# Kernel tuning notes

Hardware: AMD Instinct MI355X
Metric: run time of the kernel (lower is better)

## Reference

```python
import jax, jax.numpy as jnp
import numpy as np

THETA = 10000.0


def _rope_tables(T, head_dim, dtype):
    # w = 1/theta^(arange(1, d+1, 2)[:d//2] / d); positions start at 1 (matches source)
    exps = jnp.arange(1, head_dim + 1, 2, dtype=jnp.float32)[: head_dim // 2] / head_dim
    w = 1.0 / (THETA ** exps)
    t = jnp.arange(1, T + 1, dtype=jnp.float32)
    angles = t[:, None] * w[None, :]  # [T, d/2]
    return jnp.sin(angles).astype(dtype), jnp.cos(angles).astype(dtype)


def _rotate(x, sin, cos):
    # x: [..., T, d], sin/cos: [T, d/2]; rotate interleaved len-2 subvectors
    x1 = x[..., ::2]
    x2 = x[..., 1::2]
    x1p = x1 * cos - x2 * sin
    x2p = x1 * sin + x2 * cos
    return jnp.stack((x1p, x2p), axis=-1).reshape(x.shape)


def setup_inputs() -> dict:
    key = jax.random.key(0)
    B, Tq, Tkv, C = 4, 2048, 2048, 1024
    k1, k2, k3, k4, k5 = jax.random.split(key, 5)
    s = 1.0 / np.sqrt(C)
    return {
        "x_q": jax.random.normal(k1, (B, Tq, C), dtype=jnp.float32),
        "x_kv": jax.random.normal(k2, (B, Tkv, C), dtype=jnp.float32),
        "q_tok_mask": jnp.ones((B, Tq), dtype=bool),
        "kv_tok_mask": jnp.ones((B, Tkv), dtype=bool),
        "W_q": jax.random.normal(k3, (C, C), dtype=jnp.float32) * s,
        "W_kv": jax.random.normal(k4, (C, 2 * C), dtype=jnp.float32) * s,
        "W_c": jax.random.normal(k5, (C, C), dtype=jnp.float32) * s,
    }


def reference(x_q, x_kv, q_tok_mask, kv_tok_mask, W_q, W_kv, W_c):
    B, Tq, C = x_q.shape
    Tkv = x_kv.shape[1]
    H = 16
    D = C // H  # head_dim = 64

    q = (x_q @ W_q).reshape(B, Tq, H, D).transpose(0, 2, 1, 3)      # [B,H,Tq,D]
    kv = x_kv @ W_kv                                                  # [B,Tkv,2C]
    k, v = kv[..., :C], kv[..., C:]
    k = k.reshape(B, Tkv, H, D).transpose(0, 2, 1, 3)                 # [B,H,Tkv,D]
    v = v.reshape(B, Tkv, H, D).transpose(0, 2, 1, 3)

    sin_q, cos_q = _rope_tables(Tq, D, x_q.dtype)
    sin_k, cos_k = _rope_tables(Tkv, D, x_q.dtype)
    q = _rotate(q, sin_q, cos_q)
    k = _rotate(k, sin_k, cos_k)

    att = jnp.einsum("bhqd,bhkd->bhqk", q, k) / jnp.sqrt(jnp.asarray(D, x_q.dtype))
    mask = (q_tok_mask[:, :, None] & kv_tok_mask[:, None, :])[:, None, :, :]  # [B,1,Tq,Tkv]
    att = jnp.where(mask, att, jnp.asarray(-1e9, att.dtype))
    att = jax.nn.softmax(att, axis=-1)

    y = jnp.einsum("bhqk,bhkd->bhqd", att, v)                         # [B,H,Tq,D]
    y = y.transpose(0, 2, 1, 3).reshape(B, Tq, C)
    return y @ W_c
```

## Files before the change

kernel.cpp:

```cpp
#include <hip/hip_runtime.h>
#include <hip/hip_bf16.h>
#include <math.h>

typedef float f32x4 __attribute__((ext_vector_type(4)));
typedef short bf16x8 __attribute__((ext_vector_type(8)));

#define DEVINL __device__ __forceinline__

DEVINL unsigned short f2bf(float f) {
  unsigned int u = __float_as_uint(f);
  return (unsigned short)((u + 0x7FFFu + ((u >> 16) & 1u)) >> 16);
}
DEVINL float bf2f(unsigned short h) { return __uint_as_float(((unsigned int)h) << 16); }

DEVINL unsigned int pack_bf2(float f0, float f1) {
  unsigned int u0 = __float_as_uint(f0) + 0x8000u;
  unsigned int u1 = __float_as_uint(f1) + 0x8000u;
#if __has_builtin(__builtin_amdgcn_perm)
  return __builtin_amdgcn_perm(u1, u0, 0x07060302u);
#else
  return (u0 >> 16) | (u1 & 0xffff0000u);
#endif
}

DEVINL float fast_exp2(float x) {
#if __has_builtin(__builtin_amdgcn_exp2f)
  return __builtin_amdgcn_exp2f(x);
#else
  return exp2f(x);
#endif
}

DEVINL void glds16(const unsigned short* g, unsigned short* l) {
  __builtin_amdgcn_global_load_lds(
      (const __attribute__((address_space(1))) void*)g,
      (__attribute__((address_space(3))) void*)l, 16, 0, 0);
}

__global__ void cvt2(const float* __restrict__ a, const float* __restrict__ b,
                     unsigned short* __restrict__ da, unsigned short* __restrict__ db,
                     int n8half) {
  int halfgrid = gridDim.x >> 1;
  int hi = blockIdx.x >= halfgrid;
  const float* src = hi ? b : a;
  unsigned short* dst = hi ? db : da;
  int bx = blockIdx.x - (hi ? halfgrid : 0);
  int stride = halfgrid * blockDim.x;
  for (int i = bx * blockDim.x + threadIdx.x; i < n8half; i += stride) {
    float4 x = ((const float4*)src)[2*i];
    float4 y = ((const float4*)src)[2*i + 1];
    union { unsigned short us[8]; uint4 v; } u;
    u.us[0]=f2bf(x.x); u.us[1]=f2bf(x.y); u.us[2]=f2bf(x.z); u.us[3]=f2bf(x.w);
    u.us[4]=f2bf(y.x); u.us[5]=f2bf(y.y); u.us[6]=f2bf(y.z); u.us[7]=f2bf(y.w);
    ((uint4*)dst)[i] = u.v;
  }
}

__global__ void transpose3(const float* __restrict__ Wq, const float* __restrict__ Wkv,
                           const float* __restrict__ Wc,
                           unsigned short* __restrict__ dq, unsigned short* __restrict__ dkv,
                           unsigned short* __restrict__ dc) {
  __shared__ float tile[32][33];
  int bx = blockIdx.x;
  const float* src; unsigned short* dst; int N;
  if (bx < 32)      { src = Wq;  dst = dq;  N = 1024; }
  else if (bx < 96) { src = Wkv; dst = dkv; N = 2048; bx -= 32; }
  else              { src = Wc;  dst = dc;  N = 1024; bx -= 96; }
  const int K = 1024;
  int n0 = bx * 32, k0 = blockIdx.y * 32;
  int tx = threadIdx.x, ty = threadIdx.y;
  for (int i = 0; i < 4; ++i) {
    int k = ty + i * 8;
    tile[k][tx] = src[(long)(k0 + k) * N + n0 + tx];
  }
  __syncthreads();
  for (int i = 0; i < 4; ++i) {
    int n = ty + i * 8;
    dst[(long)(n0 + n) * K + k0 + tx] = f2bf(tile[tx][n]);
  }
}

struct GemmCtx {
  int lane, lo16, quad, wm, wn;
  int r0, soff, ldsoff, fc;
};
DEVINL void gemm_core(const unsigned short* __restrict__ A, const unsigned short* __restrict__ Bt,
                      int m0, int n0, int K,
                      unsigned short* As, unsigned short* Bs,
                      const GemmCtx& c, f32x4 acc[4][4]) {
  int aoff[4], boff[4];
  for (int mt = 0; mt < 4; ++mt) aoff[mt] = (c.wm * 64 + mt * 16 + c.lo16) * 32 + c.fc;
  for (int nt = 0; nt < 4; ++nt) boff[nt] = (c.wn * 64 + nt * 16 + c.lo16) * 32 + c.fc;
  for (int k0 = 0; k0 < K; k0 += 32) {
    glds16(A  + (long)(m0 + c.r0)      * K + k0 + c.soff, As + c.ldsoff);
    glds16(A  + (long)(m0 + 64 + c.r0) * K + k0 + c.soff, As + 2048 + c.ldsoff);
    glds16(Bt + (long)(n0 + c.r0)      * K + k0 + c.soff, Bs + c.ldsoff);
    glds16(Bt + (long)(n0 + 64 + c.r0) * K + k0 + c.soff, Bs + 2048 + c.ldsoff);
    __syncthreads();
    bf16x8 af[4], bfv[4];
    for (int mt = 0; mt < 4; ++mt) af[mt]  = *(const bf16x8*)(As + aoff[mt]);
    for (int nt = 0; nt < 4; ++nt) bfv[nt] = *(const bf16x8*)(Bs + boff[nt]);
    for (int mt = 0; mt < 4; ++mt)
      for (int nt = 0; nt < 4; ++nt)
        acc[mt][nt] = __builtin_amdgcn_mfma_f32_16x16x32_bf16(af[mt], bfv[nt], acc[mt][nt], 0, 0, 0);
    __syncthreads();
  }
}
DEVINL GemmCtx make_ctx(int tid) {
  GemmCtx c;
  int wave = tid >> 6; c.lane = tid & 63;
  c.lo16 = c.lane & 15; c.quad = c.lane >> 4;
  c.wm = wave >> 1; c.wn = wave & 1;
  c.r0 = wave * 16 + (c.lane >> 2);
  c.soff = ((c.lane & 3) ^ ((c.lane >> 3) & 3)) * 8;
  c.ldsoff = wave * 512 + c.lane * 8;
  c.fc = (c.quad ^ ((c.lo16 >> 1) & 3)) * 8;
  return c;
}

__global__ __launch_bounds__(256) void gemm_qkv(
    const unsigned short* __restrict__ xq, const unsigned short* __restrict__ xkv,
    const unsigned short* __restrict__ wq, const unsigned short* __restrict__ wkv,
    unsigned short* __restrict__ qout, unsigned short* __restrict__ kout,
    unsigned short* __restrict__ vout, float qscale) {
  __shared__ unsigned short As[128 * 32];
  __shared__ unsigned short Bs[128 * 32];
  const bool isq = blockIdx.x < 8;
  const unsigned short* A  = isq ? xq : xkv;
  const unsigned short* Bt = isq ? wq : wkv;
  const int n0 = (isq ? blockIdx.x : (blockIdx.x - 8)) * 128;
  const int m0 = blockIdx.y * 128;
  GemmCtx c = make_ctx(threadIdx.x);
  f32x4 acc[4][4];
  f32x4 zero = {0.f, 0.f, 0.f, 0.f};
  for (int i = 0; i < 4; ++i) for (int j = 0; j < 4; ++j) acc[i][j] = zero;
  gemm_core(A, Bt, m0, n0, 1024, As, Bs, c, acc);

  const bool isv = (!isq) && (n0 >= 1024);
  const float LOG2_10000_64 = 0.20762050593046f;

  if (!isv) {
    unsigned short* out = isq ? qout : kout;
    const float scale = isq ? qscale : 1.0f;
    const float sgn = (c.lo16 & 1) ? 1.0f : -1.0f;
    for (int nt = 0; nt < 4; ++nt) {
      int gn = n0 + c.wn * 64 + nt * 16 + c.lo16;
      int d = gn & 63, h = gn >> 6;
      float w = fast_exp2(-(float)(2 * (d >> 1) + 1) * LOG2_10000_64);
      for (int mt = 0; mt < 4; ++mt) {
        int gmb = m0 + c.wm * 64 + mt * 16 + c.quad * 4;
        for (int r = 0; r < 4; ++r) {
          int gm = gmb + r;
          int b = gm >> 11, t = gm & 2047;
          float v = acc[mt][nt][r];
          float p = __shfl_xor(v, 1, 64);
          float sa, ca; __sincosf((float)(t + 1) * w, &sa, &ca);
          float res = fmaf(p, sgn * sa, v * ca) * scale;
          out[((long)((b * 16 + h) * 2048 + t)) * 64 + d] = f2bf(res);
        }
      }
    }
  } else {
    for (int mt = 0; mt < 4; ++mt) {
      int gmb = m0 + c.wm * 64 + mt * 16 + c.quad * 4;
      for (int nt = 0; nt < 4; ++nt) {
        int gn = n0 + c.wn * 64 + nt * 16 + c.lo16 - 1024;
        int h = gn >> 6, d = gn & 63;
        for (int r = 0; r < 4; ++r) {
          int gm = gmb + r;
          int b = gm >> 11, t = gm & 2047;
          int u = t & 31;
          int tp = (t & ~31) | (8 * ((u >> 2) & 3) + (u & 3) + 4 * (u >> 4));
          vout[((long)((b * 16 + h) * 64 + d)) * 2048 + tp] = f2bf(acc[mt][nt][r]);
        }
      }
    }
  }
}

__global__ __launch_bounds__(256) void gemm_out(
    const unsigned short* __restrict__ A, const unsigned short* __restrict__ Bt,
    float* __restrict__ out) {
  __shared__ unsigned short As[128 * 32];
  __shared__ unsigned short Bs[128 * 32];
  const int m0 = blockIdx.y * 128, n0 = blockIdx.x * 128;
  GemmCtx c = make_ctx(threadIdx.x);
  f32x4 acc[4][4];
  f32x4 zero = {0.f, 0.f, 0.f, 0.f};
  for (int i = 0; i < 4; ++i) for (int j = 0; j < 4; ++j) acc[i][j] = zero;
  gemm_core(A, Bt, m0, n0, 1024, As, Bs, c, acc);
  for (int mt = 0; mt < 4; ++mt) {
    int gmb = m0 + c.wm * 64 + mt * 16 + c.quad * 4;
    for (int nt = 0; nt < 4; ++nt) {
      int gn = n0 + c.wn * 64 + nt * 16 + c.lo16;
      for (int r = 0; r < 4; ++r)
        out[(long)(gmb + r) * 1024 + gn] = acc[mt][nt][r];
    }
  }
}

__global__ __launch_bounds__(128, 2) void flash_st(
    const unsigned short* __restrict__ Q, const unsigned short* __restrict__ Kr,
    const unsigned short* __restrict__ Vt, unsigned short* __restrict__ Y) {
  __shared__ unsigned short Ks[64 * 64];
  __shared__ unsigned short Vs[64 * 64];
  const int tid  = threadIdx.x;
  const int wave = tid >> 6, lane = tid & 63;
  const int lo16 = lane & 15, quad = lane >> 4;
  const int bh = blockIdx.x, b = bh >> 4, h = bh & 15;
  const int q0 = blockIdx.y * 128 + wave * 64;

  bf16x8 qf[4][2];
  for (int qt = 0; qt < 4; ++qt)
    for (int dk = 0; dk < 2; ++dk)
      qf[qt][dk] = *(const bf16x8*)(Q + ((long)bh * 2048 + q0 + qt * 16 + lo16) * 64 + dk * 32 + quad * 8);

  f32x4 zero = {0.f, 0.f, 0.f, 0.f};
  f32x4 o[4][4];
  f32x4 lacc[4];
  for (int dt = 0; dt < 4; ++dt) for (int qt = 0; qt < 4; ++qt) o[dt][qt] = zero;
  for (int qt = 0; qt < 4; ++qt) lacc[qt] = zero;

  const int sr = lane >> 3;
  const int gc = ((lane & 7) ^ sr) * 8;

  for (int kb = 0; kb < 2048; kb += 64) {
    for (int p = 0; p < 4; ++p) {
      int g = p * 2 + wave;
      int r = g * 8 + sr;
      glds16(Kr + ((long)bh * 2048 + kb + r) * 64 + gc, Ks + g * 512 + lane * 8);
      glds16(Vt + ((long)bh * 64 + r) * 2048 + kb + gc, Vs + g * 512 + lane * 8);
    }
    __syncthreads();

    for (int ks = 0; ks < 2; ++ks) {
      unsigned int p2[2][4][2];
      for (int ktl = 0; ktl < 2; ++ktl) {
        const int krow = (ks * 2 + ktl) * 16 + lo16;
        const int x7 = krow & 7;
        bf16x8 ka0 = *(const bf16x8*)(Ks + krow * 64 + ((quad ^ x7) * 8));
        bf16x8 ka1 = *(const bf16x8*)(Ks + krow * 64 + (((4 + quad) ^ x7) * 8));
        for (int qt = 0; qt < 4; ++qt) {
          f32x4 s = zero;
          s = __builtin_amdgcn_mfma_f32_16x16x32_bf16(ka0, qf[qt][0], s, 0, 0, 0);
          s = __builtin_amdgcn_mfma_f32_16x16x32_bf16(ka1, qf[qt][1], s, 0, 0, 0);
          f32x4 e;
          e[0] = fast_exp2(s[0]); e[1] = fast_exp2(s[1]);
          e[2] = fast_exp2(s[2]); e[3] = fast_exp2(s[3]);
          lacc[qt] += e;
          p2[ktl][qt][0] = pack_bf2(e[0], e[1]);
          p2[ktl][qt][1] = pack_bf2(e[2], e[3]);
        }
      }
      for (int dt = 0; dt < 4; ++dt) {
        const int vrow = dt * 16 + lo16;
        bf16x8 va = *(const bf16x8*)(Vs + vrow * 64 + (((ks * 4 + quad) ^ (vrow & 7)) * 8));
        for (int qt = 0; qt < 4; ++qt) {
          union { unsigned int u[4]; bf16x8 v; } pb;
          pb.u[0] = p2[0][qt][0]; pb.u[1] = p2[0][qt][1];
          pb.u[2] = p2[1][qt][0]; pb.u[3] = p2[1][qt][1];
          o[dt][qt] = __builtin_amdgcn_mfma_f32_16x16x32_bf16(va, pb.v, o[dt][qt], 0, 0, 0);
        }
      }
    }
    __syncthreads();
  }

  float rl[4];
  for (int qt = 0; qt < 4; ++qt) {
    float l = (lacc[qt][0] + lacc[qt][1]) + (lacc[qt][2] + lacc[qt][3]);
    l += __shfl_xor(l, 16, 64);
    l += __shfl_xor(l, 32, 64);
    rl[qt] = 1.0f / l;
  }

  for (int dt = 0; dt < 4; ++dt)
    for (int qt = 0; qt < 4; ++qt) {
      float v0 = o[dt][qt][0] * rl[qt], v1 = o[dt][qt][1] * rl[qt];
      float v2 = o[dt][qt][2] * rl[qt], v3 = o[dt][qt][3] * rl[qt];
      uint2 pk; pk.x = pack_bf2(v0, v1); pk.y = pack_bf2(v2, v3);
      long row = (long)b * 2048 + q0 + qt * 16 + lo16;
      int col = h * 64 + dt * 16 + quad * 4;
      *(uint2*)(Y + row * 1024 + col) = pk;
    }
}

extern "C" void kernel_launch(void* const* d_in, const int* in_sizes, int n_in,
                              void* d_out, int out_size, void* d_ws, size_t ws_size,
                              hipStream_t stream) {
  const float* x_q  = (const float*)d_in[0];
  const float* x_kv = (const float*)d_in[1];
  const float* W_q  = (const float*)d_in[4];
  const float* W_kv = (const float*)d_in[5];
  const float* W_c  = (const float*)d_in[6];

  char* ws = (char*)d_ws;
  const size_t MB = 1u << 20;
  unsigned short* xq_bf  = (unsigned short*)(ws + 0);
  unsigned short* xkv_bf = (unsigned short*)(ws + 16 * MB);
  unsigned short* wq_t   = (unsigned short*)(ws + 32 * MB);
  unsigned short* wkv_t  = (unsigned short*)(ws + 34 * MB);
  unsigned short* wc_t   = (unsigned short*)(ws + 38 * MB);
  unsigned short* q_r    = (unsigned short*)(ws + 40 * MB);
  unsigned short* k_r    = (unsigned short*)(ws + 56 * MB);
  unsigned short* v_t    = (unsigned short*)(ws + 72 * MB);
  unsigned short* y      = xq_bf;

  const float QSCALE = 0.125f * 1.44269504088896f;

  dim3 tb(32, 8);
  cvt2<<<2048, 256, 0, stream>>>(x_q, x_kv, xq_bf, xkv_bf, 1048576);
  transpose3<<<dim3(128, 32), tb, 0, stream>>>(W_q, W_kv, W_c, wq_t, wkv_t, wc_t);
  gemm_qkv<<<dim3(24, 64), 256, 0, stream>>>(xq_bf, xkv_bf, wq_t, wkv_t, q_r, k_r, v_t, QSCALE);
  flash_st<<<dim3(64, 16), 128, 0, stream>>>(q_r, k_r, v_t, y);
  gemm_out<<<dim3(8, 64), 256, 0, stream>>>(y, wc_t, (float*)d_out);
}
```

Baseline: 314.8 us.

## Double-buffer K/V tiles in flash attention with async prefetch and MFMA priority

Splits the K and V shared-memory tiles into two buffers and issues the loads for the next key block before computing the current one. Explicit vmcnt waits and raw barriers replace __syncthreads so global-to-LDS traffic can overlap the MFMA and exp work. It also raises wave priority around MFMA groups. The cost is twice the LDS, which may limit occupancy, and the hand-written vmcnt(8) must match the number of outstanding loads per stage.

```diff
diff --git a/kernel.cpp b/kernel.cpp
--- a/kernel.cpp
+++ b/kernel.cpp
@@ -202,8 +202,8 @@
 __global__ __launch_bounds__(128, 2) void flash_st(
     const unsigned short* __restrict__ Q, const unsigned short* __restrict__ Kr,
     const unsigned short* __restrict__ Vt, unsigned short* __restrict__ Y) {
-  __shared__ unsigned short Ks[64 * 64];
-  __shared__ unsigned short Vs[64 * 64];
+  __shared__ unsigned short Ks[2][64 * 64];
+  __shared__ unsigned short Vs[2][64 * 64];
   const int tid  = threadIdx.x;
   const int wave = tid >> 6, lane = tid & 63;
   const int lo16 = lane & 15, quad = lane >> 4;
@@ -223,27 +223,45 @@
 
   const int sr = lane >> 3;
   const int gc = ((lane & 7) ^ sr) * 8;
+  const unsigned short* Kg = Kr + (long)bh * 2048 * 64;
+  const unsigned short* Vg = Vt + (long)bh * 64 * 2048;
+
+#define STAGE_KV(KB, BI) do {                                            \
+    for (int p = 0; p < 4; ++p) {                                        \
+      int g = p * 2 + wave;                                              \
+      int r = g * 8 + sr;                                                \
+      glds16(Kg + (long)((KB) + r) * 64 + gc, &Ks[BI][g * 512 + lane * 8]); \
+      glds16(Vg + (long)r * 2048 + (KB) + gc, &Vs[BI][g * 512 + lane * 8]); \
+    } } while (0)
+
+  STAGE_KV(0, 0);
+  int buf = 0;
 
   for (int kb = 0; kb < 2048; kb += 64) {
-    for (int p = 0; p < 4; ++p) {
-      int g = p * 2 + wave;
-      int r = g * 8 + sr;
-      glds16(Kr + ((long)bh * 2048 + kb + r) * 64 + gc, Ks + g * 512 + lane * 8);
-      glds16(Vt + ((long)bh * 64 + r) * 2048 + kb + gc, Vs + g * 512 + lane * 8);
-    }
-    __syncthreads();
+    if (kb + 64 < 2048) {
+      STAGE_KV(kb + 64, buf ^ 1);
+      asm volatile("s_waitcnt vmcnt(8)" ::: "memory");
+    } else {
+      asm volatile("s_waitcnt vmcnt(0)" ::: "memory");
+    }
+    __builtin_amdgcn_s_barrier();
+    asm volatile("" ::: "memory");
+    const unsigned short* Kb = &Ks[buf][0];
+    const unsigned short* Vb = &Vs[buf][0];
 
     for (int ks = 0; ks < 2; ++ks) {
       unsigned int p2[2][4][2];
       for (int ktl = 0; ktl < 2; ++ktl) {
         const int krow = (ks * 2 + ktl) * 16 + lo16;
         const int x7 = krow & 7;
-        bf16x8 ka0 = *(const bf16x8*)(Ks + krow * 64 + ((quad ^ x7) * 8));
-        bf16x8 ka1 = *(const bf16x8*)(Ks + krow * 64 + (((4 + quad) ^ x7) * 8));
+        bf16x8 ka0 = *(const bf16x8*)(Kb + krow * 64 + ((quad ^ x7) * 8));
+        bf16x8 ka1 = *(const bf16x8*)(Kb + krow * 64 + (((4 + quad) ^ x7) * 8));
         for (int qt = 0; qt < 4; ++qt) {
           f32x4 s = zero;
+          __builtin_amdgcn_s_setprio(1);
           s = __builtin_amdgcn_mfma_f32_16x16x32_bf16(ka0, qf[qt][0], s, 0, 0, 0);
           s = __builtin_amdgcn_mfma_f32_16x16x32_bf16(ka1, qf[qt][1], s, 0, 0, 0);
+          __builtin_amdgcn_s_setprio(0);
           f32x4 e;
           e[0] = fast_exp2(s[0]); e[1] = fast_exp2(s[1]);
           e[2] = fast_exp2(s[2]); e[3] = fast_exp2(s[3]);
@@ -254,17 +272,22 @@
       }
       for (int dt = 0; dt < 4; ++dt) {
         const int vrow = dt * 16 + lo16;
-        bf16x8 va = *(const bf16x8*)(Vs + vrow * 64 + (((ks * 4 + quad) ^ (vrow & 7)) * 8));
+        bf16x8 va = *(const bf16x8*)(Vb + vrow * 64 + (((ks * 4 + quad) ^ (vrow & 7)) * 8));
+        __builtin_amdgcn_s_setprio(1);
         for (int qt = 0; qt < 4; ++qt) {
           union { unsigned int u[4]; bf16x8 v; } pb;
           pb.u[0] = p2[0][qt][0]; pb.u[1] = p2[0][qt][1];
           pb.u[2] = p2[1][qt][0]; pb.u[3] = p2[1][qt][1];
           o[dt][qt] = __builtin_amdgcn_mfma_f32_16x16x32_bf16(va, pb.v, o[dt][qt], 0, 0, 0);
         }
+        __builtin_amdgcn_s_setprio(0);
       }
     }
-    __syncthreads();
-  }
+    asm volatile("" ::: "memory");
+    __builtin_amdgcn_s_barrier();
+    buf ^= 1;
+  }
+#undef STAGE_KV
 
   float rl[4];
   for (int qt = 0; qt < 4; ++qt) {
```

Result: no change. 318.2 us (+1.1%).

## Load K/V fragments directly from global into registers, drop LDS staging

Applied to the files above, without the earlier changes.

The flash attention kernel no longer stages K and V tiles through shared memory with barriers. Each wave now loads its MFMA operand fragments straight from global memory into registers, relying on L2/L1 for reuse between the two waves. It also adds s_setprio around MFMA groups and removes the occupancy hint from launch_bounds. This removes LDS traffic and __syncthreads. The cost is duplicated global loads across waves, less coalesced access for the strided V reads, and higher register pressure.

```diff
diff --git a/kernel.cpp b/kernel.cpp
--- a/kernel.cpp
+++ b/kernel.cpp
@@ -199,17 +199,18 @@
   }
 }
 
-__global__ __launch_bounds__(128, 2) void flash_st(
+__global__ __launch_bounds__(128) void flash_st(
     const unsigned short* __restrict__ Q, const unsigned short* __restrict__ Kr,
     const unsigned short* __restrict__ Vt, unsigned short* __restrict__ Y) {
-  __shared__ unsigned short Ks[64 * 64];
-  __shared__ unsigned short Vs[64 * 64];
   const int tid  = threadIdx.x;
   const int wave = tid >> 6, lane = tid & 63;
   const int lo16 = lane & 15, quad = lane >> 4;
   const int bh = blockIdx.x, b = bh >> 4, h = bh & 15;
   const int q0 = blockIdx.y * 128 + wave * 64;
 
+  const unsigned short* Kg = Kr + (long)bh * 2048 * 64;
+  const unsigned short* Vg = Vt + (long)bh * 64 * 2048;
+
   bf16x8 qf[4][2];
   for (int qt = 0; qt < 4; ++qt)
     for (int dk = 0; dk < 2; ++dk)
@@ -221,29 +222,29 @@
   for (int dt = 0; dt < 4; ++dt) for (int qt = 0; qt < 4; ++qt) o[dt][qt] = zero;
   for (int qt = 0; qt < 4; ++qt) lacc[qt] = zero;
 
-  const int sr = lane >> 3;
-  const int gc = ((lane & 7) ^ sr) * 8;
+  const unsigned short* kp = Kg + (long)lo16 * 64 + quad * 8;
+  const unsigned short* vp = Vg + (long)lo16 * 2048 + quad * 8;
 
   for (int kb = 0; kb < 2048; kb += 64) {
-    for (int p = 0; p < 4; ++p) {
-      int g = p * 2 + wave;
-      int r = g * 8 + sr;
-      glds16(Kr + ((long)bh * 2048 + kb + r) * 64 + gc, Ks + g * 512 + lane * 8);
-      glds16(Vt + ((long)bh * 64 + r) * 2048 + kb + gc, Vs + g * 512 + lane * 8);
-    }
-    __syncthreads();
+    bf16x8 ka[4][2];
+    bf16x8 va[2][4];
+    for (int kt = 0; kt < 4; ++kt)
+      for (int hf = 0; hf < 2; ++hf)
+        ka[kt][hf] = *(const bf16x8*)(kp + (long)(kb + kt * 16) * 64 + hf * 32);
+    for (int ks = 0; ks < 2; ++ks)
+      for (int dt = 0; dt < 4; ++dt)
+        va[ks][dt] = *(const bf16x8*)(vp + (long)(dt * 16) * 2048 + kb + ks * 32);
 
     for (int ks = 0; ks < 2; ++ks) {
       unsigned int p2[2][4][2];
       for (int ktl = 0; ktl < 2; ++ktl) {
-        const int krow = (ks * 2 + ktl) * 16 + lo16;
-        const int x7 = krow & 7;
-        bf16x8 ka0 = *(const bf16x8*)(Ks + krow * 64 + ((quad ^ x7) * 8));
-        bf16x8 ka1 = *(const bf16x8*)(Ks + krow * 64 + (((4 + quad) ^ x7) * 8));
+        const int kt = ks * 2 + ktl;
         for (int qt = 0; qt < 4; ++qt) {
           f32x4 s = zero;
-          s = __builtin_amdgcn_mfma_f32_16x16x32_bf16(ka0, qf[qt][0], s, 0, 0, 0);
-          s = __builtin_amdgcn_mfma_f32_16x16x32_bf16(ka1, qf[qt][1], s, 0, 0, 0);
+          __builtin_amdgcn_s_setprio(1);
+          s = __builtin_amdgcn_mfma_f32_16x16x32_bf16(ka[kt][0], qf[qt][0], s, 0, 0, 0);
+          s = __builtin_amdgcn_mfma_f32_16x16x32_bf16(ka[kt][1], qf[qt][1], s, 0, 0, 0);
+          __builtin_amdgcn_s_setprio(0);
           f32x4 e;
           e[0] = fast_exp2(s[0]); e[1] = fast_exp2(s[1]);
           e[2] = fast_exp2(s[2]); e[3] = fast_exp2(s[3]);
@@ -253,17 +254,16 @@
         }
       }
       for (int dt = 0; dt < 4; ++dt) {
-        const int vrow = dt * 16 + lo16;
-        bf16x8 va = *(const bf16x8*)(Vs + vrow * 64 + (((ks * 4 + quad) ^ (vrow & 7)) * 8));
+        __builtin_amdgcn_s_setprio(1);
         for (int qt = 0; qt < 4; ++qt) {
           union { unsigned int u[4]; bf16x8 v; } pb;
           pb.u[0] = p2[0][qt][0]; pb.u[1] = p2[0][qt][1];
           pb.u[2] = p2[1][qt][0]; pb.u[3] = p2[1][qt][1];
-          o[dt][qt] = __builtin_amdgcn_mfma_f32_16x16x32_bf16(va, pb.v, o[dt][qt], 0, 0, 0);
+          o[dt][qt] = __builtin_amdgcn_mfma_f32_16x16x32_bf16(va[ks][dt], pb.v, o[dt][qt], 0, 0, 0);
         }
+        __builtin_amdgcn_s_setprio(0);
       }
     }
-    __syncthreads();
   }
 
   float rl[4];
```

Result: slower. 359.7 us (+14.3%).
